# Kernel tuning notes

Measured on AMD Instinct MI355X. Metric: run time of the kernel, lower is better.

The kernel has to match this reference:

```python
import jax, jax.numpy as jnp
import numpy as np

N_ENT = 50000   # entities (nodes)
N_REL = 500     # relations
DEG = 32        # regular in-degree of the full KG
TOPK = 10       # topk in-edges kept per node by dgl.sampling.select_topk
H_DIM = 256
N_HEADS = 4
HEAD_DIM = H_DIM // N_HEADS
NEG_SLOPE = 0.2


def _leaky(x):
    return jnp.where(x >= 0, x, NEG_SLOPE * x)


def setup_inputs() -> dict:
    key = jax.random.key(0)
    ks = jax.random.split(key, 8)
    s = 0.05
    return {
        'ent_emb': jax.random.normal(ks[0], (N_ENT, H_DIM), dtype=jnp.float32),
        'rel_emb': jax.random.normal(ks[1], (N_REL, H_DIM), dtype=jnp.float32),
        'W': jax.random.normal(ks[2], (N_HEADS, H_DIM, HEAD_DIM), dtype=jnp.float32) * s,
        'W_r': jax.random.normal(ks[3], (N_HEADS, H_DIM, HEAD_DIM), dtype=jnp.float32) * s,
        'a': jax.random.normal(ks[4], (N_HEADS, 3 * HEAD_DIM), dtype=jnp.float32) * s,
        'neigh_w': jax.random.normal(ks[5], (H_DIM, H_DIM), dtype=jnp.float32) * s,
        'src': jax.random.randint(ks[6], (N_ENT, DEG), 0, N_ENT),   # src node of each in-edge of node n
        'rel_id': jax.random.randint(ks[7], (N_ENT, DEG), 0, N_REL),
    }


def reference(ent_emb, rel_emb, W, W_r, a, neigh_w, src, rel_id):
    # ---- head-0 scores used for top-k in-edge sampling (select_topk, edge_dir='in') ----
    emb_t0 = ent_emb @ W[0]          # [N, hd]
    rel_t0 = rel_emb @ W_r[0]        # [R, hd]
    a0 = a[0]
    # concat([src,dst,rel]) @ a  ==  src@a_src + dst@a_dst + rel@a_rel
    s_src = emb_t0 @ a0[:HEAD_DIM]                 # [N]
    s_dst = emb_t0 @ a0[HEAD_DIM:2 * HEAD_DIM]     # [N]
    s_rel = rel_t0 @ a0[2 * HEAD_DIM:]             # [R]
    score0 = _leaky(s_src[src] + s_dst[:, None] + s_rel[rel_id])   # [N, DEG]
    _, top_idx = jax.lax.top_k(score0, TOPK)                        # [N, K]
    src_sel = jnp.take_along_axis(src, top_idx, axis=1)             # [N, K]
    rel_sel = jnp.take_along_axis(rel_id, top_idx, axis=1)          # [N, K]

    # ---- all heads on the sampled subgraph (vectorized over heads) ----
    emb_t = jnp.einsum('nd,hde->hne', ent_emb, W)     # [H, N, hd]
    rel_t = jnp.einsum('rd,hde->hre', rel_emb, W_r)   # [H, R, hd]
    a3 = a.reshape(N_HEADS, 3, HEAD_DIM)
    ss = jnp.einsum('hne,he->hn', emb_t, a3[:, 0])    # [H, N]
    sd = jnp.einsum('hne,he->hn', emb_t, a3[:, 1])    # [H, N]
    sr = jnp.einsum('hre,he->hr', rel_t, a3[:, 2])    # [H, R]
    scores = _leaky(ss[:, src_sel] + sd[:, :, None] + sr[:, rel_sel])  # [H, N, K]
    norm = jax.nn.softmax(scores, axis=-1)            # edge-softmax over in-edges per dst

    # comp_op == 'add' : u_add_e, weighted by attention, summed into dst
    comp = emb_t[:, src_sel] + rel_t[:, rel_sel]      # [H, N, K, hd]
    neigh = jnp.einsum('hnke,hnk->hne', comp, norm)   # [H, N, hd]

    neigh = jnp.transpose(neigh, (1, 0, 2)).reshape(ent_emb.shape[0], H_DIM)  # concat heads
    return jnp.tanh(neigh @ neigh_w)                  # bn disabled (cfg.bn=False)
```

## Files before the change

### kernel.cpp

```cpp
#include <hip/hip_runtime.h>
#include <math.h>

#define N_ENT 50000
#define N_REL 500
#define DEG 32
#define TOPK 10
#define H_DIM 256
#define N_HEADS 4
#define HEAD_DIM 64

typedef __attribute__((ext_vector_type(8))) short short8v;
typedef __attribute__((ext_vector_type(4))) float f32x4;

constexpr size_t OFF_SSRC0 = 0;
constexpr size_t OFF_SR0   = 400000;
constexpr size_t OFF_U0    = 404000;
constexpr size_t OFF_V0    = 406048;
constexpr size_t OFF_SS    = 408096;
constexpr size_t OFF_SSR   = 2008096;
constexpr size_t OFF_U8    = 2024096;
constexpr size_t OFF_V8    = 2032288;
constexpr size_t OFF_B1H   = 2040480;
constexpr size_t OFF_B2H   = 2302624;
constexpr size_t OFF_B3H   = 2564768;
constexpr size_t OFF_RPK   = 2826912;
constexpr size_t OFF_EAH   = 3089056;
constexpr size_t OFF_EMBBF = 28713632;
constexpr size_t OFF_RELBF = 54313632;
constexpr size_t WS_NEED   = 54569632;

__device__ __forceinline__ float leaky(float x) { return x >= 0.f ? x : 0.2f * x; }

__device__ __forceinline__ unsigned short bf16_rne(float x) {
    unsigned int u = __float_as_uint(x);
    unsigned int r = u + 0x7fffu + ((u >> 16) & 1u);
    return (unsigned short)(r >> 16);
}
__device__ __forceinline__ float bf2f(unsigned short x) {
    return __uint_as_float((unsigned)x << 16);
}

__device__ __forceinline__ size_t pack_off(int row, int d) {
    return ((size_t)(row >> 4) * 8 + (d >> 5)) * 512 +
           (((d >> 3) & 3) * 16 + (row & 15)) * 8 + (d & 7);
}

__global__ __launch_bounds__(256) void setup_kernel(
    const float* __restrict__ W, const float* __restrict__ W_r,
    const float* __restrict__ a, const float* __restrict__ nw,
    float* __restrict__ U8, double* __restrict__ u0,
    float* __restrict__ V8, double* __restrict__ v0,
    unsigned short* __restrict__ b1h, unsigned short* __restrict__ b2h,
    unsigned short* __restrict__ b3h)
{
    const int bid = blockIdx.x;
    const int tid = threadIdx.x;
    if (bid == 0) {
        int d = tid;
        #pragma unroll
        for (int h = 0; h < N_HEADS; ++h) {
            float ss = 0.f, sd = 0.f;
            #pragma unroll
            for (int e = 0; e < HEAD_DIM; ++e) {
                float w = W[h * 16384 + d * 64 + e];
                ss += w * a[h * 192 + e];
                sd += w * a[h * 192 + 64 + e];
            }
            U8[d * 8 + h] = ss;
            U8[d * 8 + 4 + h] = sd;
        }
        double s0 = 0.0;
        #pragma unroll
        for (int e = 0; e < HEAD_DIM; ++e)
            s0 += (double)W[d * 64 + e] * (double)a[e];
        u0[d] = s0;
    } else if (bid == 1) {
        int d = tid;
        #pragma unroll
        for (int h = 0; h < N_HEADS; ++h) {
            float sv = 0.f;
            #pragma unroll
            for (int e = 0; e < HEAD_DIM; ++e)
                sv += W_r[h * 16384 + d * 64 + e] * a[h * 192 + 128 + e];
            V8[d * 8 + h] = sv;
            V8[d * 8 + 4 + h] = 0.f;
        }
        double s0 = 0.0;
        #pragma unroll
        for (int e = 0; e < HEAD_DIM; ++e)
            s0 += (double)W_r[d * 64 + e] * (double)a[128 + e];
        v0[d] = s0;
    } else {
        int n = bid - 2;
        int k = tid;
        int h = n >> 6, e = n & 63;
        float x1 = W[h * 16384 + k * 64 + e];
        float x2 = nw[k * 256 + n];
        float x3 = W_r[h * 16384 + k * 64 + e];
        size_t off = pack_off(n, k);
        b1h[off] = bf16_rne(x1);
        b2h[off] = bf16_rne(x2);
        b3h[off] = bf16_rne(x3);
    }
}

__global__ __launch_bounds__(256) void ss_kernel(
    const float* __restrict__ ent, const float* __restrict__ relm,
    const float* __restrict__ U8, const double* __restrict__ u0,
    const float* __restrict__ V8, const double* __restrict__ v0,
    float* __restrict__ SS, double* __restrict__ ssrc0, unsigned short* __restrict__ apk,
    float* __restrict__ SSR, double* __restrict__ sr0, unsigned short* __restrict__ rpk)
{
    const int tid = threadIdx.x;
    const int l = tid & 63;
    const int el = l & 31;
    const int q2 = l >> 5;

    const bool isent = blockIdx.x < 2048;
    const float* X = isent ? ent : relm;
    const float* U8v = isent ? U8 : V8;
    const double* u0v = isent ? u0 : v0;
    float* SSout = isent ? SS : SSR;
    double* s0out = isent ? ssrc0 : sr0;
    unsigned short* Xpk = isent ? apk : rpk;
    const int N = isent ? N_ENT : N_REL;
    const int wave0 = isent ? ((blockIdx.x * 256 + tid) >> 6)
                            : (((blockIdx.x - 2048) * 256 + tid) >> 6);
    const int nwaves = isent ? 8192 : 252;

    float uu[8][8];
    #pragma unroll
    for (int i = 0; i < 8; ++i) {
        float4 a4 = *(const float4*)(U8v + (el * 8 + i) * 8);
        float4 b4 = *(const float4*)(U8v + (el * 8 + i) * 8 + 4);
        uu[i][0] = a4.x; uu[i][1] = a4.y; uu[i][2] = a4.z; uu[i][3] = a4.w;
        uu[i][4] = b4.x; uu[i][5] = b4.y; uu[i][6] = b4.z; uu[i][7] = b4.w;
    }
    double ud[8];
    #pragma unroll
    for (int i = 0; i < 8; ++i) ud[i] = u0v[el * 8 + i];

    const int jout = ((el & 1) << 2) | (el & 2) | ((el >> 2) & 1);
    const int half = N / 2;

    int p = wave0;
    float4 x1, x2;
    if (p < half) {
        int n0 = p * 2 + q2;
        x1 = *(const float4*)(X + (size_t)n0 * 256 + el * 8);
        x2 = *(const float4*)(X + (size_t)n0 * 256 + el * 8 + 4);
    }
    for (; p < half; p += nwaves) {
        const int n = p * 2 + q2;
        const float4 cx1 = x1, cx2 = x2;
        const int np = p + nwaves;
        if (np < half) {
            int n1 = np * 2 + q2;
            x1 = *(const float4*)(X + (size_t)n1 * 256 + el * 8);
            x2 = *(const float4*)(X + (size_t)n1 * 256 + el * 8 + 4);
        }
        float xs[8] = {cx1.x, cx1.y, cx1.z, cx1.w, cx2.x, cx2.y, cx2.z, cx2.w};

        short8v ov;
        #pragma unroll
        for (int i = 0; i < 8; ++i) ov[i] = (short)bf16_rne(xs[i]);
        *(short8v*)(Xpk + pack_off(n, el * 8)) = ov;

        float pj[8] = {0.f, 0.f, 0.f, 0.f, 0.f, 0.f, 0.f, 0.f};
        double pd = 0.0;
        #pragma unroll
        for (int i = 0; i < 8; ++i) {
            #pragma unroll
            for (int j = 0; j < 8; ++j) pj[j] += xs[i] * uu[i][j];
            pd += (double)xs[i] * ud[i];
        }

        const bool b1 = (el & 1);
        float q[4];
        #pragma unroll
        for (int j = 0; j < 4; ++j) {
            float mine = b1 ? pj[j + 4] : pj[j];
            float send = b1 ? pj[j] : pj[j + 4];
            q[j] = mine + __shfl_xor(send, 1);
        }
        const bool b2 = (el & 2);
        float r2[2];
        #pragma unroll
        for (int j = 0; j < 2; ++j) {
            float mine = b2 ? q[j + 2] : q[j];
            float send = b2 ? q[j] : q[j + 2];
            r2[j] = mine + __shfl_xor(send, 2);
        }
        const bool b4 = (el & 4);
        {
            float mine = b4 ? r2[1] : r2[0];
            float send = b4 ? r2[0] : r2[1];
            r2[0] = mine + __shfl_xor(send, 4);
        }
        r2[0] += __shfl_xor(r2[0], 8);
        r2[0] += __shfl_xor(r2[0], 16);

        #pragma unroll
        for (int off = 1; off < 32; off <<= 1) pd += __shfl_xor(pd, off);

        if (el < 8) SSout[(size_t)n * 8 + jout] = r2[0];
        if (el == 0) s0out[n] = pd;
    }
}

__global__ __launch_bounds__(256, 4) void gemm_hi(
    const unsigned short* __restrict__ A1, const unsigned short* __restrict__ B1,
    unsigned short* __restrict__ C1, int M1, int nb1,
    const unsigned short* __restrict__ A2, const unsigned short* __restrict__ B2,
    unsigned short* __restrict__ C2, int M2)
{
    const int tid = threadIdx.x;
    const int l = tid & 63;
    const int w = tid >> 6;
    const int rl = l & 15;
    const int ql = l >> 4;

    const int b = blockIdx.x;
    const unsigned short* Apk = (b < nb1) ? A1 : A2;
    const unsigned short* Bh  = (b < nb1) ? B1 : B2;
    unsigned short* C         = (b < nb1) ? C1 : C2;
    const int M               = (b < nb1) ? M1 : M2;
    const int bm              = ((b < nb1) ? b : (b - nb1)) * 64;

    const unsigned short* ab = Apk + (size_t)(bm >> 4) * 4096 + l * 8;
    const unsigned short* bhb = Bh + (size_t)w * 16384 + l * 8;

    f32x4 acc[4][4];
    #pragma unroll
    for (int i = 0; i < 4; ++i)
        #pragma unroll
        for (int j = 0; j < 4; ++j) acc[i][j] = (f32x4){0.f, 0.f, 0.f, 0.f};

    #pragma unroll
    for (int ks = 0; ks < 8; ++ks) {
        short8v ah[4], bh[4];
        #pragma unroll
        for (int mf = 0; mf < 4; ++mf)
            ah[mf] = *(const short8v*)(ab + mf * 4096 + ks * 512);
        #pragma unroll
        for (int nf = 0; nf < 4; ++nf)
            bh[nf] = *(const short8v*)(bhb + nf * 4096 + ks * 512);
        #pragma unroll
        for (int mf = 0; mf < 4; ++mf)
            #pragma unroll
            for (int nf = 0; nf < 4; ++nf)
                acc[mf][nf] = __builtin_amdgcn_mfma_f32_16x16x32_bf16(ah[mf], bh[nf], acc[mf][nf], 0, 0, 0);
    }

    #pragma unroll
    for (int mf = 0; mf < 4; ++mf) {
        int row0 = bm + mf * 16 + ql * 4;
        #pragma unroll
        for (int nf = 0; nf < 4; ++nf) {
            int c = w * 64 + nf * 16 + rl;
            #pragma unroll
            for (int j = 0; j < 4; ++j) {
                int r = row0 + j;
                if (r < M)
                    C[(size_t)r * 256 + c] = bf16_rne(acc[mf][nf][j]);
            }
        }
    }
}

__global__ __launch_bounds__(256, 3) void node_kernel(
    const int* __restrict__ src, const int* __restrict__ relid,
    const float* __restrict__ SS, const double* __restrict__ ssrc0,
    const float* __restrict__ SSR, const double* __restrict__ sr0,
    const unsigned short* __restrict__ emb_bf, const unsigned short* __restrict__ rel_bf,
    unsigned short* __restrict__ napk)
{
    __shared__ double scs[8][33];
    __shared__ unsigned idsS[8][12];
    __shared__ float wtsS[8][10][4];
    __shared__ float sumsS[8][4];

    const int tid = threadIdx.x;
    const int l = tid & 63;
    const int el = l & 31;
    const int hb = l & 32;
    const int nib = tid >> 5;
    const int n = blockIdx.x * 8 + nib;

    const int sd_ = src[n * DEG + el];
    const int rd_ = relid[n * DEG + el];
    const double sc0 = ssrc0[sd_] + sr0[rd_];
    scs[nib][el] = sc0;

    int cnt = 0;
    #pragma unroll
    for (int j = 0; j < DEG; ++j) {
        double sj = scs[nib][j];
        cnt += (sj > sc0 || (sj == sc0 && j < el)) ? 1 : 0;
    }
    const bool sel = (cnt < TOPK);
    const unsigned mask = (unsigned)(__ballot(sel) >> hb);
    const int pos = __popc(mask & ((1u << el) - 1u));

    float ex = 0.f, ey = 0.f, ez = 0.f, ew = 0.f;
    if (sel) {
        float4 ssv = *(const float4*)(SS + (size_t)sd_ * 8);
        float4 srv = *(const float4*)(SSR + (size_t)rd_ * 8);
        float4 sdv = *(const float4*)(SS + (size_t)n * 8 + 4);
        ex = __expf(leaky(ssv.x + sdv.x + srv.x));
        ey = __expf(leaky(ssv.y + sdv.y + srv.y));
        ez = __expf(leaky(ssv.z + sdv.z + srv.z));
        ew = __expf(leaky(ssv.w + sdv.w + srv.w));
        idsS[nib][pos] = (unsigned)sd_ | ((unsigned)rd_ << 16);
        float4 wv; wv.x = ex; wv.y = ey; wv.z = ez; wv.w = ew;
        *(float4*)&wtsS[nib][pos][0] = wv;
    }

    float p0, p1;
    {
        const bool b1 = (el & 1);
        float m0 = b1 ? ez : ex, s0 = b1 ? ex : ez;
        float m1 = b1 ? ew : ey, s1 = b1 ? ey : ew;
        p0 = m0 + __shfl_xor(s0, 1);
        p1 = m1 + __shfl_xor(s1, 1);
    }
    float qsum;
    {
        const bool b2 = (el & 2);
        float m = b2 ? p1 : p0, s = b2 ? p0 : p1;
        qsum = m + __shfl_xor(s, 2);
    }
    qsum += __shfl_xor(qsum, 4);
    qsum += __shfl_xor(qsum, 8);
    qsum += __shfl_xor(qsum, 16);
    if (el < 4) sumsS[nib][((el & 1) << 1) | ((el >> 1) & 1)] = qsum;

    const int h = el >> 3;

    int skA[TOPK], rkA[TOPK];
    #pragma unroll
    for (int k = 0; k < TOPK; ++k) {
        unsigned idk = idsS[nib][k];
        skA[k] = (int)(idk & 0xFFFFu);
        rkA[k] = (int)(idk >> 16);
    }

    short8v ev[TOPK], rv[TOPK];
    #pragma unroll
    for (int k = 0; k < TOPK; ++k)
        ev[k] = *(const short8v*)(emb_bf + (size_t)skA[k] * 256 + el * 8);
    #pragma unroll
    for (int k = 0; k < TOPK; ++k)
        rv[k] = *(const short8v*)(rel_bf + (size_t)rkA[k] * 256 + el * 8);
    asm volatile("s_waitcnt vmcnt(0)" ::: "memory");

    const float rsh = 1.f / sumsS[nib][h];
    float acc[8] = {0.f, 0.f, 0.f, 0.f, 0.f, 0.f, 0.f, 0.f};
    #pragma unroll
    for (int k = 0; k < TOPK; ++k) {
        float w = wtsS[nib][k][h] * rsh;
        #pragma unroll
        for (int j = 0; j < 8; ++j)
            acc[j] += w * (bf2f((unsigned short)ev[k][j]) + bf2f((unsigned short)rv[k][j]));
    }

    short8v ov;
    #pragma unroll
    for (int j = 0; j < 8; ++j) ov[j] = (short)bf16_rne(acc[j]);
    *(short8v*)(napk + pack_off(n, el * 8)) = ov;
}

__global__ __launch_bounds__(256, 4) void gemm_out(
    const unsigned short* __restrict__ Apk, const unsigned short* __restrict__ Bpkh,
    float* __restrict__ Cout, int M)
{
    const int tid = threadIdx.x;
    const int l = tid & 63;
    const int w = tid >> 6;
    const int bm = blockIdx.x * 64;
    const int rl = l & 15;
    const int ql = l >> 4;

    const unsigned short* ab = Apk + (size_t)(bm >> 4) * 4096 + l * 8;
    const unsigned short* bhb = Bpkh + (size_t)w * 16384 + l * 8;

    f32x4 acc[4][4];
    #pragma unroll
    for (int i = 0; i < 4; ++i)
        #pragma unroll
        for (int j = 0; j < 4; ++j) acc[i][j] = (f32x4){0.f, 0.f, 0.f, 0.f};

    #pragma unroll
    for (int ks = 0; ks < 8; ++ks) {
        short8v ah[4], bh[4];
        #pragma unroll
        for (int mf = 0; mf < 4; ++mf)
            ah[mf] = *(const short8v*)(ab + mf * 4096 + ks * 512);
        #pragma unroll
        for (int nf = 0; nf < 4; ++nf)
            bh[nf] = *(const short8v*)(bhb + nf * 4096 + ks * 512);
        #pragma unroll
        for (int mf = 0; mf < 4; ++mf)
            #pragma unroll
            for (int nf = 0; nf < 4; ++nf)
                acc[mf][nf] = __builtin_amdgcn_mfma_f32_16x16x32_bf16(ah[mf], bh[nf], acc[mf][nf], 0, 0, 0);
    }

    #pragma unroll
    for (int mf = 0; mf < 4; ++mf) {
        int row0 = bm + mf * 16 + ql * 4;
        #pragma unroll
        for (int nf = 0; nf < 4; ++nf) {
            int c = w * 64 + nf * 16 + rl;
            #pragma unroll
            for (int j = 0; j < 4; ++j) {
                int r = row0 + j;
                if (r < M) {
                    float v = acc[mf][nf][j];
                    Cout[(size_t)r * 256 + c] = 1.f - 2.f / (__expf(2.f * v) + 1.f);
                }
            }
        }
    }
}

extern "C" void kernel_launch(void* const* d_in, const int* in_sizes, int n_in,
                              void* d_out, int out_size, void* d_ws, size_t ws_size,
                              hipStream_t stream) {
    const float* ent  = (const float*)d_in[0];
    const float* rel  = (const float*)d_in[1];
    const float* W    = (const float*)d_in[2];
    const float* W_r  = (const float*)d_in[3];
    const float* a    = (const float*)d_in[4];
    const float* nw   = (const float*)d_in[5];
    const int*   srcp = (const int*)d_in[6];
    const int*   ridp = (const int*)d_in[7];
    float* out = (float*)d_out;

    if (ws_size < WS_NEED) return;

    char* ws = (char*)d_ws;
    double* ssrc0 = (double*)(ws + OFF_SSRC0);
    double* sr0   = (double*)(ws + OFF_SR0);
    double* u0    = (double*)(ws + OFF_U0);
    double* v0    = (double*)(ws + OFF_V0);
    float*  SS    = (float*)(ws + OFF_SS);
    float*  SSR   = (float*)(ws + OFF_SSR);
    float*  U8    = (float*)(ws + OFF_U8);
    float*  V8    = (float*)(ws + OFF_V8);
    unsigned short* b1h = (unsigned short*)(ws + OFF_B1H);
    unsigned short* b2h = (unsigned short*)(ws + OFF_B2H);
    unsigned short* b3h = (unsigned short*)(ws + OFF_B3H);
    unsigned short* rpk = (unsigned short*)(ws + OFF_RPK);
    unsigned short* apk = (unsigned short*)(ws + OFF_EAH);
    unsigned short* embbf = (unsigned short*)(ws + OFF_EMBBF);
    unsigned short* relbf = (unsigned short*)(ws + OFF_RELBF);
    unsigned short* napk = apk;

    setup_kernel<<<258, 256, 0, stream>>>(W, W_r, a, nw, U8, u0, V8, v0,
                                          b1h, b2h, b3h);
    ss_kernel<<<2111, 256, 0, stream>>>(ent, rel, U8, u0, V8, v0,
                                        SS, ssrc0, apk, SSR, sr0, rpk);
    gemm_hi<<<790, 256, 0, stream>>>(apk, b1h, embbf, N_ENT, 782,
                                     rpk, b3h, relbf, N_REL);
    node_kernel<<<6250, 256, 0, stream>>>(srcp, ridp, SS, ssrc0, SSR, sr0,
                                          embbf, relbf, napk);
    gemm_out<<<782, 256, 0, stream>>>(napk, b2h, out, N_ENT);
}
```

Before: 146.3 us.

## Store GEMM A operands row-major and stage them through LDS

The producer kernels now write the bf16 activation matrices in plain row-major order instead of the MFMA-fragment packed layout. The two GEMM kernels load each 64x256 A tile cooperatively into padded shared memory and read fragments from there. This aims to make producer stores and GEMM loads contiguous and coalesced. In exchange it adds an LDS round-trip, a barrier and about 33KB of shared memory per block, which may reduce occupancy.

```diff
diff --git a/kernel.cpp b/kernel.cpp
--- a/kernel.cpp
+++ b/kernel.cpp
@@ -164,7 +164,7 @@
         short8v ov;
         #pragma unroll
         for (int i = 0; i < 8; ++i) ov[i] = (short)bf16_rne(xs[i]);
-        *(short8v*)(Xpk + pack_off(n, el * 8)) = ov;
+        *(short8v*)(Xpk + (size_t)n * 256 + el * 8) = ov;
 
         float pj[8] = {0.f, 0.f, 0.f, 0.f, 0.f, 0.f, 0.f, 0.f};
         double pd = 0.0;
@@ -214,6 +214,8 @@
     const unsigned short* __restrict__ A2, const unsigned short* __restrict__ B2,
     unsigned short* __restrict__ C2, int M2)
 {
+    __shared__ unsigned short As[64][264];
+
     const int tid = threadIdx.x;
     const int l = tid & 63;
     const int w = tid >> 6;
@@ -221,13 +223,21 @@
     const int ql = l >> 4;
 
     const int b = blockIdx.x;
-    const unsigned short* Apk = (b < nb1) ? A1 : A2;
-    const unsigned short* Bh  = (b < nb1) ? B1 : B2;
-    unsigned short* C         = (b < nb1) ? C1 : C2;
-    const int M               = (b < nb1) ? M1 : M2;
-    const int bm              = ((b < nb1) ? b : (b - nb1)) * 64;
-
-    const unsigned short* ab = Apk + (size_t)(bm >> 4) * 4096 + l * 8;
+    const unsigned short* A = (b < nb1) ? A1 : A2;
+    const unsigned short* Bh = (b < nb1) ? B1 : B2;
+    unsigned short* C       = (b < nb1) ? C1 : C2;
+    const int M             = (b < nb1) ? M1 : M2;
+    const int bm            = ((b < nb1) ? b : (b - nb1)) * 64;
+
+    const unsigned short* Ag = A + (size_t)bm * 256;
+    #pragma unroll
+    for (int i = 0; i < 8; ++i) {
+        int u = i * 256 + tid;
+        short8v v = *(const short8v*)(Ag + (size_t)u * 8);
+        *(short8v*)&As[u >> 5][(u & 31) * 8] = v;
+    }
+    __syncthreads();
+
     const unsigned short* bhb = Bh + (size_t)w * 16384 + l * 8;
 
     f32x4 acc[4][4];
@@ -241,7 +251,7 @@
         short8v ah[4], bh[4];
         #pragma unroll
         for (int mf = 0; mf < 4; ++mf)
-            ah[mf] = *(const short8v*)(ab + mf * 4096 + ks * 512);
+            ah[mf] = *(const short8v*)&As[mf * 16 + rl][ks * 32 + ql * 8];
         #pragma unroll
         for (int nf = 0; nf < 4; ++nf)
             bh[nf] = *(const short8v*)(bhb + nf * 4096 + ks * 512);
@@ -367,13 +377,15 @@
     short8v ov;
     #pragma unroll
     for (int j = 0; j < 8; ++j) ov[j] = (short)bf16_rne(acc[j]);
-    *(short8v*)(napk + pack_off(n, el * 8)) = ov;
+    *(short8v*)(napk + (size_t)n * 256 + el * 8) = ov;
 }
 
 __global__ __launch_bounds__(256, 4) void gemm_out(
-    const unsigned short* __restrict__ Apk, const unsigned short* __restrict__ Bpkh,
+    const unsigned short* __restrict__ A, const unsigned short* __restrict__ Bpkh,
     float* __restrict__ Cout, int M)
 {
+    __shared__ unsigned short As[64][264];
+
     const int tid = threadIdx.x;
     const int l = tid & 63;
     const int w = tid >> 6;
@@ -381,7 +393,15 @@
     const int rl = l & 15;
     const int ql = l >> 4;
 
-    const unsigned short* ab = Apk + (size_t)(bm >> 4) * 4096 + l * 8;
+    const unsigned short* Ag = A + (size_t)bm * 256;
+    #pragma unroll
+    for (int i = 0; i < 8; ++i) {
+        int u = i * 256 + tid;
+        short8v v = *(const short8v*)(Ag + (size_t)u * 8);
+        *(short8v*)&As[u >> 5][(u & 31) * 8] = v;
+    }
+    __syncthreads();
+
     const unsigned short* bhb = Bpkh + (size_t)w * 16384 + l * 8;
 
     f32x4 acc[4][4];
@@ -395,7 +415,7 @@
         short8v ah[4], bh[4];
         #pragma unroll
         for (int mf = 0; mf < 4; ++mf)
-            ah[mf] = *(const short8v*)(ab + mf * 4096 + ks * 512);
+            ah[mf] = *(const short8v*)&As[mf * 16 + rl][ks * 32 + ql * 8];
         #pragma unroll
         for (int nf = 0; nf < 4; ++nf)
             bh[nf] = *(const short8v*)(bhb + nf * 4096 + ks * 512);
```

After: 140.7 us. -3.8%, faster.
